# Performance work log

Measured on AMD Instinct MI355X. Metric: run time of the kernel, lower is better.

## Reference

```python
import jax, jax.numpy as jnp
import numpy as np

N = 100000
E = 1600000
B = 64
NUM_CLASSES = 10


def setup_inputs() -> dict:
    key = jax.random.key(0)
    ks = jax.random.split(key, 8)
    x = jax.random.normal(ks[0], (N, 5), dtype=jnp.float32)
    edge_index = jax.random.randint(ks[1], (2, E), 0, N, dtype=jnp.int64)
    batch = jnp.sort(jax.random.randint(ks[2], (N,), 0, B, dtype=jnp.int64))

    def glorot(k, fan_in, fan_out):
        s = jnp.sqrt(6.0 / (fan_in + fan_out)).astype(jnp.float32)
        return jax.random.uniform(k, (fan_in, fan_out), jnp.float32, -s, s)

    dims = [(5, 32), (32, 64), (64, 128), (128, 256)]
    Ws = [glorot(jax.random.fold_in(ks[3], i), a, b) for i, (a, b) in enumerate(dims)]
    bs = [jnp.zeros((b,), jnp.float32) for (_, b) in dims]
    fc1_w = glorot(ks[4], 256, 100)
    fc1_b = jnp.zeros((100,), jnp.float32)
    fc2_w = glorot(ks[5], 100, NUM_CLASSES)
    fc2_b = jnp.zeros((NUM_CLASSES,), jnp.float32)
    return {
        'x': x, 'edge_index': edge_index, 'batch': batch,
        'W1': Ws[0], 'b1': bs[0], 'W2': Ws[1], 'b2': bs[1],
        'W3': Ws[2], 'b3': bs[2], 'W4': Ws[3], 'b4': bs[3],
        'fc1_w': fc1_w, 'fc1_b': fc1_b, 'fc2_w': fc2_w, 'fc2_b': fc2_b,
    }


def _gcn_conv(x, W, b, src, dst, dinv):
    h = x @ W                                   # [N, out]
    norm = (dinv[src] * dinv[dst])[:, None]      # [E, 1]
    msg = h[src] * norm                          # gather + scale
    agg = jax.ops.segment_sum(msg, dst, num_segments=N)
    agg = agg + h * (dinv * dinv)[:, None]       # self-loop contribution
    return agg + b


def reference(x, edge_index, batch, W1, b1, W2, b2, W3, b3, W4, b4,
              fc1_w, fc1_b, fc2_w, fc2_b):
    src, dst = edge_index[0], edge_index[1]
    # degree including self-loop
    deg = jax.ops.segment_sum(jnp.ones((E,), jnp.float32), dst, num_segments=N) + 1.0
    dinv = jax.lax.rsqrt(deg)

    h = jax.nn.relu(_gcn_conv(x, W1, b1, src, dst, dinv))
    # mesh_unpool with pool target 0 -> identity
    h = jax.nn.relu(_gcn_conv(h, W2, b2, src, dst, dinv))
    h = jax.nn.relu(_gcn_conv(h, W3, b3, src, dst, dinv))
    h = jax.nn.relu(_gcn_conv(h, W4, b4, src, dst, dinv))

    # global mean pool over graphs
    sums = jax.ops.segment_sum(h, batch, num_segments=B)
    cnt = jax.ops.segment_sum(jnp.ones((N,), jnp.float32), batch, num_segments=B)
    pooled = sums / jnp.maximum(cnt, 1.0)[:, None]

    h = jax.nn.relu(pooled @ fc1_w + fc1_b)
    return jax.nn.log_softmax(h @ fc2_w + fc2_b, axis=-1)
```

## Files before the change

kernel.cpp:

```cpp
#include <hip/hip_runtime.h>
#include <hip/hip_bf16.h>
#include <cmath>

#define NN 100000
#define NE 1600000
#define NBATCH 64
#define NB 391
#define NBP 512
#define BCAP 5120
#define NPAD (NB * BCAP)

typedef __attribute__((ext_vector_type(8))) _Float16 f16x8;
typedef __attribute__((ext_vector_type(4))) float f32x4;
typedef __attribute__((ext_vector_type(2))) float f32x2;

__device__ __forceinline__ void atomAdd(float* p, float v) {
  unsafeAtomicAdd(p, v);
}

__device__ __forceinline__ unsigned char f2fp8(float f) {
  int pk = __builtin_amdgcn_cvt_pk_fp8_f32(f, f, 0, false);
  return (unsigned char)(pk & 0xff);
}

__global__ __launch_bounds__(256) void k_bin(const int* __restrict__ src,
    const int* __restrict__ dst, int* __restrict__ bucketCnt, unsigned* __restrict__ pairs,
    const float* __restrict__ W2, const float* __restrict__ W3, const float* __restrict__ W4,
    _Float16* __restrict__ Wt2, _Float16* __restrict__ Wt3, _Float16* __restrict__ Wt4) {
  __shared__ int hist[NBP];
  __shared__ int scn[NBP];
  __shared__ int ofs[NBP];
  __shared__ int gbase[NBP];
  __shared__ unsigned buf[4096];
  __shared__ unsigned short bufb[4096];
  const int base = blockIdx.x * 4096;
  const int n = (NE - base < 4096) ? NE - base : 4096;
  for (int i = threadIdx.x; i < NBP; i += 256) hist[i] = 0;
  __syncthreads();

  int myS[16], myD[16];
  int nloc = 0;
  for (int i = threadIdx.x, j = 0; i < n; i += 256, ++j) {
    myS[j] = src[base + i];
    myD[j] = dst[base + i];
    atomicAdd(&hist[myD[j] >> 8], 1);
    nloc = j + 1;
  }
  __syncthreads();

  scn[threadIdx.x] = hist[threadIdx.x];
  scn[threadIdx.x + 256] = hist[threadIdx.x + 256];
  __syncthreads();
  for (int off = 1; off < NBP; off <<= 1) {
    const int i0 = threadIdx.x, i1 = threadIdx.x + 256;
    int t0 = (i0 >= off) ? scn[i0 - off] : 0;
    int t1 = (i1 >= off) ? scn[i1 - off] : 0;
    __syncthreads();
    scn[i0] += t0;
    scn[i1] += t1;
    __syncthreads();
  }
  ofs[threadIdx.x] = scn[threadIdx.x] - hist[threadIdx.x];
  ofs[threadIdx.x + 256] = scn[threadIdx.x + 256] - hist[threadIdx.x + 256];
  for (int b = threadIdx.x; b < NB; b += 256) {
    int c = hist[b];
    if (c) gbase[b] = b * BCAP + atomicAdd(&bucketCnt[b], c);
  }
  __syncthreads();

  for (int j = 0; j < nloc; ++j) {
    int b = myD[j] >> 8;
    int slot = atomicAdd(&ofs[b], 1);
    buf[slot] = ((unsigned)myS[j] << 8) | ((unsigned)myD[j] & 255u);
    bufb[slot] = (unsigned short)b;
  }
  __syncthreads();

  for (int i = threadIdx.x; i < n; i += 256) {
    int b = (int)bufb[i];
    int ex = scn[b] - hist[b];
    pairs[gbase[b] + (i - ex)] = buf[i];
  }

  int idx = blockIdx.x * 256 + threadIdx.x;
  if (idx < 2048) {
    int k = idx / 64, m = idx - k * 64;
    Wt2[m * 32 + k] = (_Float16)W2[idx];
  } else if (idx < 10240) {
    int j = idx - 2048;
    int k = j / 128, m = j - k * 128;
    Wt3[m * 64 + k] = (_Float16)W3[j];
  } else if (idx < 43008) {
    int j = idx - 10240;
    int k = j / 256, m = j - k * 256;
    Wt4[m * 128 + k] = (_Float16)W4[j];
  }
}

__global__ __launch_bounds__(256) void k_cntfill(const unsigned* __restrict__ pairs,
    const int* __restrict__ bucketCnt, const int* __restrict__ batch,
    const float* __restrict__ x, int* __restrict__ rowbeg, int* __restrict__ rowend,
    float* __restrict__ dinv, int* __restrict__ csrc, float* __restrict__ pcnt,
    _Float16* __restrict__ xs8) {
  __shared__ int c[256];
  __shared__ int scn[256];
  __shared__ int rowb[256];
  __shared__ int ofs[256];
  __shared__ int h[64];
  const int tid = threadIdx.x;
  c[tid] = 0; ofs[tid] = 0;
  if (tid < 64) h[tid] = 0;
  __syncthreads();
  const int b = blockIdx.x;
  const int s = b * BCAP;
  const int e = s + bucketCnt[b];
  for (int i = s + tid; i < e; i += 256) atomicAdd(&c[pairs[i] & 255u], 1);
  __syncthreads();
  const int v = c[tid];
  scn[tid] = v;
  __syncthreads();
  for (int off = 1; off < 256; off <<= 1) {
    int t = (tid >= off) ? scn[tid - off] : 0;
    __syncthreads();
    scn[tid] += t;
    __syncthreads();
  }
  rowb[tid] = s + scn[tid] - v;
  const int node = b * 256 + tid;
  rowbeg[node] = rowb[tid];
  rowend[node] = rowb[tid] + v;
  if (node < NN) {
    const float di = rsqrtf((float)v + 1.0f);
    dinv[node] = di;
    f16x8 o = {0, 0, 0, 0, 0, 0, 0, 0};
    o[0] = (_Float16)(x[(size_t)node * 5 + 0] * di);
    o[1] = (_Float16)(x[(size_t)node * 5 + 1] * di);
    o[2] = (_Float16)(x[(size_t)node * 5 + 2] * di);
    o[3] = (_Float16)(x[(size_t)node * 5 + 3] * di);
    o[4] = (_Float16)(x[(size_t)node * 5 + 4] * di);
    *(f16x8*)(xs8 + (size_t)node * 8) = o;
    atomicAdd(&h[batch[node]], 1);
  }
  __syncthreads();
  for (int i = s + tid; i < e; i += 256) {
    unsigned p = pairs[i];
    int t = (int)(p & 255u);
    int pos = rowb[t] + atomicAdd(&ofs[t], 1);
    csrc[pos] = (int)(p >> 8);
  }
  if (tid < 64 && h[tid]) atomAdd(&pcnt[tid], (float)h[tid]);
}

struct MegaArgs {
  const _Float16* xs8;
  const int* rowbeg; const int* rowend; const int* csrc;
  const float* dinv;
  const float* W1; const float* b1;
  unsigned char* F0;
  const _Float16* Wt2; const float* b2;
  unsigned char* F1;
  const _Float16* Wt3; const float* b3;
  unsigned char* F2;
  const _Float16* Wt4; const float* b4;
  _Float16* AG;
  const int* batch; float* pooled; const float* pcnt;
  const float* fc1w; const float* fc1b; const float* fc2w; const float* fc2b;
  float* out;
};

__global__ __launch_bounds__(256) void kw_l1(MegaArgs a) {
  __shared__ float w_s[160];
  __shared__ float b_s[32];
  const int tid = threadIdx.x;
  if (tid < 160) w_s[tid] = a.W1[tid];
  if (tid < 32) b_s[tid] = a.b1[tid];
  __syncthreads();
  const int r = blockIdx.x * 256 + tid;
  if (r >= NN) return;
  const float di = a.dinv[r];
  f16x8 av = *(const f16x8*)(a.xs8 + (size_t)r * 8);
  f16x8 cacc = {0, 0, 0, 0, 0, 0, 0, 0};
  int e = a.rowbeg[r];
  const int e1 = a.rowend[r];
  for (; e + 2 <= e1; e += 2) {
    const int s0 = a.csrc[e], s1 = a.csrc[e + 1];
    av   += *(const f16x8*)(a.xs8 + (size_t)s0 * 8);
    cacc += *(const f16x8*)(a.xs8 + (size_t)s1 * 8);
  }
  if (e < e1) av += *(const f16x8*)(a.xs8 + (size_t)a.csrc[e] * 8);
  av += cacc;
  const float f0 = (float)av[0] * di, f1 = (float)av[1] * di, f2 = (float)av[2] * di,
              f3 = (float)av[3] * di, f4 = (float)av[4] * di;
  float v[32];
#pragma unroll
  for (int j = 0; j < 32; ++j) {
    float s = b_s[j] + f0 * w_s[j] + f1 * w_s[32 + j] + f2 * w_s[64 + j]
                     + f3 * w_s[96 + j] + f4 * w_s[128 + j];
    v[j] = fmaxf(s, 0.f) * di;
  }
  unsigned u[8];
#pragma unroll
  for (int g2 = 0; g2 < 8; ++g2) {
    int uu = 0;
    uu = __builtin_amdgcn_cvt_pk_fp8_f32(v[4 * g2],     v[4 * g2 + 1], uu, false);
    uu = __builtin_amdgcn_cvt_pk_fp8_f32(v[4 * g2 + 2], v[4 * g2 + 3], uu, true);
    u[g2] = (unsigned)uu;
  }
  uint4* op = (uint4*)(a.F0 + (size_t)r * 32);
  op[0] = make_uint4(u[0], u[1], u[2], u[3]);
  op[1] = make_uint4(u[4], u[5], u[6], u[7]);
}

template<int K>
__global__ __launch_bounds__(256) void kw_gather8(const unsigned char* __restrict__ in,
    MegaArgs a) {
  constexpr int TPR = K / 16;
  constexpr int RPB = 256 / TPR;
  const int r = blockIdx.x * RPB + threadIdx.x / TPR;
  if (r >= NN) return;
  const int c = (threadIdx.x % TPR) * 16;
  const float di = a.dinv[r];
  f32x2 acc[8];
  {
    const uint4 v = *(const uint4*)(in + (size_t)r * K + c);
    acc[0] = __builtin_amdgcn_cvt_pk_f32_fp8(v.x, false);
    acc[1] = __builtin_amdgcn_cvt_pk_f32_fp8(v.x, true);
    acc[2] = __builtin_amdgcn_cvt_pk_f32_fp8(v.y, false);
    acc[3] = __builtin_amdgcn_cvt_pk_f32_fp8(v.y, true);
    acc[4] = __builtin_amdgcn_cvt_pk_f32_fp8(v.z, false);
    acc[5] = __builtin_amdgcn_cvt_pk_f32_fp8(v.z, true);
    acc[6] = __builtin_amdgcn_cvt_pk_f32_fp8(v.w, false);
    acc[7] = __builtin_amdgcn_cvt_pk_f32_fp8(v.w, true);
  }
  int e = a.rowbeg[r];
  const int e1 = a.rowend[r];
  for (; e + 2 <= e1; e += 2) {
    const int s0 = a.csrc[e], s1 = a.csrc[e + 1];
    const uint4 v0 = *(const uint4*)(in + (size_t)s0 * K + c);
    const uint4 v1 = *(const uint4*)(in + (size_t)s1 * K + c);
    acc[0] += __builtin_amdgcn_cvt_pk_f32_fp8(v0.x, false);
    acc[1] += __builtin_amdgcn_cvt_pk_f32_fp8(v0.x, true);
    acc[2] += __builtin_amdgcn_cvt_pk_f32_fp8(v0.y, false);
    acc[3] += __builtin_amdgcn_cvt_pk_f32_fp8(v0.y, true);
    acc[4] += __builtin_amdgcn_cvt_pk_f32_fp8(v0.z, false);
    acc[5] += __builtin_amdgcn_cvt_pk_f32_fp8(v0.z, true);
    acc[6] += __builtin_amdgcn_cvt_pk_f32_fp8(v0.w, false);
    acc[7] += __builtin_amdgcn_cvt_pk_f32_fp8(v0.w, true);
    acc[0] += __builtin_amdgcn_cvt_pk_f32_fp8(v1.x, false);
    acc[1] += __builtin_amdgcn_cvt_pk_f32_fp8(v1.x, true);
    acc[2] += __builtin_amdgcn_cvt_pk_f32_fp8(v1.y, false);
    acc[3] += __builtin_amdgcn_cvt_pk_f32_fp8(v1.y, true);
    acc[4] += __builtin_amdgcn_cvt_pk_f32_fp8(v1.z, false);
    acc[5] += __builtin_amdgcn_cvt_pk_f32_fp8(v1.z, true);
    acc[6] += __builtin_amdgcn_cvt_pk_f32_fp8(v1.w, false);
    acc[7] += __builtin_amdgcn_cvt_pk_f32_fp8(v1.w, true);
  }
  if (e < e1) {
    const uint4 v0 = *(const uint4*)(in + (size_t)a.csrc[e] * K + c);
    acc[0] += __builtin_amdgcn_cvt_pk_f32_fp8(v0.x, false);
    acc[1] += __builtin_amdgcn_cvt_pk_f32_fp8(v0.x, true);
    acc[2] += __builtin_amdgcn_cvt_pk_f32_fp8(v0.y, false);
    acc[3] += __builtin_amdgcn_cvt_pk_f32_fp8(v0.y, true);
    acc[4] += __builtin_amdgcn_cvt_pk_f32_fp8(v0.z, false);
    acc[5] += __builtin_amdgcn_cvt_pk_f32_fp8(v0.z, true);
    acc[6] += __builtin_amdgcn_cvt_pk_f32_fp8(v0.w, false);
    acc[7] += __builtin_amdgcn_cvt_pk_f32_fp8(v0.w, true);
  }
  _Float16 o[16];
#pragma unroll
  for (int j = 0; j < 8; ++j) {
    o[2 * j]     = (_Float16)(acc[j].x * di);
    o[2 * j + 1] = (_Float16)(acc[j].y * di);
  }
  uint4* op = (uint4*)(a.AG + (size_t)r * K + c);
  op[0] = *(uint4*)&o[0];
  op[1] = *(uint4*)&o[8];
}

template<int K, int M, int MODE>
__global__ __launch_bounds__(256) void kw_gemm(MegaArgs a,
    const _Float16* __restrict__ Wt, const float* __restrict__ bias,
    unsigned char* __restrict__ outp) {
  constexpr int KC = 32;
  constexpr int KP = K + 8;
  constexpr int WP = KC + 8;
  constexpr int CTW = M / 64;
  constexpr int C8 = K / 8;
  __shared__ _Float16 a_s[64 * KP];
  __shared__ _Float16 w_s[M * WP];
  const int tid = threadIdx.x;
  const int wave = tid >> 6, lane = tid & 63;
  const int m16 = lane & 15, q = lane >> 4;
  const int r0 = blockIdx.x * 64;

  for (int idx = tid; idx < 64 * C8; idx += 256) {
    int row = idx / C8, cc = (idx % C8) * 8;
    uint4 v = {0u, 0u, 0u, 0u};
    if (r0 + row < NN) v = *(const uint4*)(a.AG + (size_t)(r0 + row) * K + cc);
    *(uint4*)&a_s[row * KP + cc] = v;
  }
  f32x4 acc[4][CTW];
#pragma unroll
  for (int rt = 0; rt < 4; ++rt)
#pragma unroll
    for (int ct = 0; ct < CTW; ++ct) acc[rt][ct] = (f32x4){0.f, 0.f, 0.f, 0.f};

  for (int kc = 0; kc < K; kc += KC) {
    __syncthreads();
    for (int idx = tid; idx < M * (KC / 8); idx += 256) {
      int m = idx / (KC / 8), cc = (idx % (KC / 8)) * 8;
      uint4 v = *(const uint4*)(Wt + (size_t)m * K + kc + cc);
      *(uint4*)&w_s[m * WP + cc] = v;
    }
    __syncthreads();
    f16x8 bfr[CTW];
#pragma unroll
    for (int ct = 0; ct < CTW; ++ct)
      bfr[ct] = *(const f16x8*)&w_s[(wave * (M / 4) + ct * 16 + m16) * WP + q * 8];
#pragma unroll
    for (int rt = 0; rt < 4; ++rt) {
      f16x8 afr = *(const f16x8*)&a_s[(rt * 16 + m16) * KP + kc + q * 8];
#pragma unroll
      for (int ct = 0; ct < CTW; ++ct)
        acc[rt][ct] = __builtin_amdgcn_mfma_f32_16x16x32_f16(afr, bfr[ct], acc[rt][ct], 0, 0, 0);
    }
  }

  if constexpr (MODE == 1) {
    const int rlast = (r0 + 63 < NN) ? r0 + 63 : NN - 1;
    const int bmin = a.batch[r0];
    const int bmax = a.batch[rlast];
    int rowb[4][4];
#pragma unroll
    for (int rt = 0; rt < 4; ++rt)
#pragma unroll
      for (int reg = 0; reg < 4; ++reg) {
        const int row = r0 + rt * 16 + q * 4 + reg;
        rowb[rt][reg] = (row < NN) ? a.batch[row] : -1;
      }
#pragma unroll
    for (int ct = 0; ct < CTW; ++ct) {
      const int col = wave * (M / 4) + ct * 16 + m16;
      const float bv = bias[col];
      for (int b = bmin; b <= bmax; ++b) {
        float s = 0.f;
#pragma unroll
        for (int rt = 0; rt < 4; ++rt)
#pragma unroll
          for (int reg = 0; reg < 4; ++reg)
            if (rowb[rt][reg] == b) s += fmaxf(acc[rt][ct][reg] + bv, 0.f);
        s += __shfl_xor(s, 16);
        s += __shfl_xor(s, 32);
        if (q == 0) atomAdd(&a.pooled[b * M + col], s);
      }
    }
  } else {
    float dsc[4][4];
#pragma unroll
    for (int rt = 0; rt < 4; ++rt)
#pragma unroll
      for (int reg = 0; reg < 4; ++reg) {
        const int row = r0 + rt * 16 + q * 4 + reg;
        dsc[rt][reg] = (row < NN) ? a.dinv[row] : 0.f;
      }
#pragma unroll
    for (int rt = 0; rt < 4; ++rt) {
#pragma unroll
      for (int ct = 0; ct < CTW; ++ct) {
        const int col = wave * (M / 4) + ct * 16 + m16;
        const float bv = bias[col];
#pragma unroll
        for (int reg = 0; reg < 4; ++reg) {
          const int row = r0 + rt * 16 + q * 4 + reg;
          if (row < NN) {
            float vv = fmaxf(acc[rt][ct][reg] + bv, 0.f) * dsc[rt][reg];
            outp[(size_t)row * M + col] = f2fp8(vv);
          }
        }
      }
    }
  }
}

__global__ __launch_bounds__(256) void kw_mlp(MegaArgs a) {
  __shared__ float p[256];
  __shared__ float h1[100];
  __shared__ float lo[10];
  const int tid = threadIdx.x;
  const int b = blockIdx.x;
  const float inv = 1.0f / fmaxf(a.pcnt[b], 1.0f);
  p[tid] = a.pooled[b * 256 + tid] * inv;
  __syncthreads();
  for (int j = tid; j < 100; j += 256) {
    float s = a.fc1b[j];
    for (int k = 0; k < 256; ++k) s += p[k] * a.fc1w[k * 100 + j];
    h1[j] = fmaxf(s, 0.f);
  }
  __syncthreads();
  if (tid < 10) {
    float s = a.fc2b[tid];
    for (int k = 0; k < 100; ++k) s += h1[k] * a.fc2w[k * 10 + tid];
    lo[tid] = s;
  }
  __syncthreads();
  if (tid == 0) {
    float m = lo[0];
    for (int j = 1; j < 10; ++j) m = fmaxf(m, lo[j]);
    float ssum = 0.f;
    for (int j = 0; j < 10; ++j) ssum += expf(lo[j] - m);
    float lse = m + logf(ssum);
    for (int j = 0; j < 10; ++j) a.out[b * 10 + j] = lo[j] - lse;
  }
}

extern "C" void kernel_launch(void* const* d_in, const int* in_sizes, int n_in,
                              void* d_out, int out_size, void* d_ws, size_t ws_size,
                              hipStream_t stream) {
  const float* x     = (const float*)d_in[0];
  const int*   ei    = (const int*)d_in[1];
  const int*   batch = (const int*)d_in[2];
  const float* W1 = (const float*)d_in[3];  const float* b1 = (const float*)d_in[4];
  const float* W2 = (const float*)d_in[5];  const float* b2 = (const float*)d_in[6];
  const float* W3 = (const float*)d_in[7];  const float* b3 = (const float*)d_in[8];
  const float* W4 = (const float*)d_in[9];  const float* b4 = (const float*)d_in[10];
  const float* fc1w = (const float*)d_in[11]; const float* fc1b = (const float*)d_in[12];
  const float* fc2w = (const float*)d_in[13]; const float* fc2b = (const float*)d_in[14];
  float* out = (float*)d_out;

  const int* src = ei;
  const int* dst = ei + NE;

  float* ws = (float*)d_ws;
  float* pooled = ws;
  float* pcnt   = pooled + 16384;
  int*   bucketCnt = (int*)(pcnt + 64);
  float* dinv   = (float*)(bucketCnt + 512);
  int*   rowbeg = (int*)(dinv + 100352);
  int*   rowend = rowbeg + 100352;
  int*   csrc   = rowend + 100352;
  unsigned* pairs = (unsigned*)(csrc + NPAD);
  _Float16* xs8 = (_Float16*)(pairs + NPAD);
  unsigned char* F0 = (unsigned char*)(xs8 + 800768);
  unsigned char* F1 = F0 + (size_t)NN * 32;
  unsigned char* F2 = F1 + (size_t)NN * 64;
  _Float16* AG  = (_Float16*)(F2 + (size_t)NN * 128);
  _Float16* Wt2 = AG + (size_t)NN * 128;
  _Float16* Wt3 = Wt2 + 32 * 64;
  _Float16* Wt4 = Wt3 + 64 * 128;

  (void)hipMemsetAsync(pooled, 0, (16384 + 64 + 512) * sizeof(float), stream);
  k_bin<<<(NE + 4095) / 4096, 256, 0, stream>>>(src, dst, bucketCnt, pairs,
                                                W2, W3, W4, Wt2, Wt3, Wt4);
  k_cntfill<<<NB, 256, 0, stream>>>(pairs, bucketCnt, batch, x,
                                    rowbeg, rowend, dinv, csrc, pcnt, xs8);

  MegaArgs m;
  m.xs8 = xs8; m.rowbeg = rowbeg; m.rowend = rowend; m.csrc = csrc;
  m.dinv = dinv;
  m.W1 = W1; m.b1 = b1; m.F0 = F0;
  m.Wt2 = Wt2; m.b2 = b2; m.F1 = F1;
  m.Wt3 = Wt3; m.b3 = b3; m.F2 = F2;
  m.Wt4 = Wt4; m.b4 = b4; m.AG = AG;
  m.batch = batch; m.pooled = pooled; m.pcnt = pcnt;
  m.fc1w = fc1w; m.fc1b = fc1b; m.fc2w = fc2w; m.fc2b = fc2b;
  m.out = out;

  kw_l1<<<(NN + 255) / 256, 256, 0, stream>>>(m);
  kw_gather8<32><<<(NN + 127) / 128, 256, 0, stream>>>(F0, m);
  kw_gemm<32, 64, 0><<<(NN + 63) / 64, 256, 0, stream>>>(m, Wt2, b2, F1);
  kw_gather8<64><<<(NN + 63) / 64, 256, 0, stream>>>(F1, m);
  kw_gemm<64, 128, 0><<<(NN + 63) / 64, 256, 0, stream>>>(m, Wt3, b3, F2);
  kw_gather8<128><<<(NN + 31) / 32, 256, 0, stream>>>(F2, m);
  kw_gemm<128, 256, 1><<<(NN + 63) / 64, 256, 0, stream>>>(m, Wt4, b4, nullptr);
  kw_mlp<<<NBATCH, 256, 0, stream>>>(m);
}
```

Baseline: 285.8 us.

## Store aggregated features in FP8 and fuse MLP head into final GEMM

The gather kernel now writes its aggregated features as packed FP8 instead of FP16, halving the intermediate traffic between gather and GEMM. The GEMM converts FP8 back to FP16 when loading into shared memory. The final GEMM uses a done counter and a release flag so its first 64 blocks spin-wait and then run the MLP and log-softmax, which removes the separate kw_mlp launch. Zeroing of pooled moves into kw_l1, shrinking the memset. Risks are extra FP8 precision loss and possible deadlock if the waiting blocks stay resident while later blocks cannot be scheduled.

```diff
diff --git a/kernel.cpp b/kernel.cpp
--- a/kernel.cpp
+++ b/kernel.cpp
@@ -9,6 +9,7 @@
 #define NBP 512
 #define BCAP 5120
 #define NPAD (NB * BCAP)
+#define FLAG_MAGIC 0x1234567
 
 typedef __attribute__((ext_vector_type(8))) _Float16 f16x8;
 typedef __attribute__((ext_vector_type(4))) float f32x4;
@@ -21,6 +22,18 @@
 __device__ __forceinline__ unsigned char f2fp8(float f) {
   int pk = __builtin_amdgcn_cvt_pk_fp8_f32(f, f, 0, false);
   return (unsigned char)(pk & 0xff);
+}
+
+__device__ __forceinline__ void fp8x16_to_f16(uint4 v, _Float16* h) {
+  f32x2 t;
+  t = __builtin_amdgcn_cvt_pk_f32_fp8(v.x, false); h[0] = (_Float16)t.x;  h[1] = (_Float16)t.y;
+  t = __builtin_amdgcn_cvt_pk_f32_fp8(v.x, true);  h[2] = (_Float16)t.x;  h[3] = (_Float16)t.y;
+  t = __builtin_amdgcn_cvt_pk_f32_fp8(v.y, false); h[4] = (_Float16)t.x;  h[5] = (_Float16)t.y;
+  t = __builtin_amdgcn_cvt_pk_f32_fp8(v.y, true);  h[6] = (_Float16)t.x;  h[7] = (_Float16)t.y;
+  t = __builtin_amdgcn_cvt_pk_f32_fp8(v.z, false); h[8] = (_Float16)t.x;  h[9] = (_Float16)t.y;
+  t = __builtin_amdgcn_cvt_pk_f32_fp8(v.z, true);  h[10] = (_Float16)t.x; h[11] = (_Float16)t.y;
+  t = __builtin_amdgcn_cvt_pk_f32_fp8(v.w, false); h[12] = (_Float16)t.x; h[13] = (_Float16)t.y;
+  t = __builtin_amdgcn_cvt_pk_f32_fp8(v.w, true);  h[14] = (_Float16)t.x; h[15] = (_Float16)t.y;
 }
 
 __global__ __launch_bounds__(256) void k_bin(const int* __restrict__ src,
@@ -162,8 +175,9 @@
   const _Float16* Wt3; const float* b3;
   unsigned char* F2;
   const _Float16* Wt4; const float* b4;
-  _Float16* AG;
+  unsigned char* AG8;
   const int* batch; float* pooled; const float* pcnt;
+  int* done; int* flag;
   const float* fc1w; const float* fc1b; const float* fc2w; const float* fc2b;
   float* out;
 };
@@ -172,6 +186,7 @@
   __shared__ float w_s[160];
   __shared__ float b_s[32];
   const int tid = threadIdx.x;
+  if (blockIdx.x < 64) a.pooled[blockIdx.x * 256 + tid] = 0.f;
   if (tid < 160) w_s[tid] = a.W1[tid];
   if (tid < 32) b_s[tid] = a.b1[tid];
   __syncthreads();
@@ -266,15 +281,17 @@
     acc[6] += __builtin_amdgcn_cvt_pk_f32_fp8(v0.w, false);
     acc[7] += __builtin_amdgcn_cvt_pk_f32_fp8(v0.w, true);
   }
-  _Float16 o[16];
-#pragma unroll
-  for (int j = 0; j < 8; ++j) {
-    o[2 * j]     = (_Float16)(acc[j].x * di);
-    o[2 * j + 1] = (_Float16)(acc[j].y * di);
-  }
-  uint4* op = (uint4*)(a.AG + (size_t)r * K + c);
-  op[0] = *(uint4*)&o[0];
-  op[1] = *(uint4*)&o[8];
+  int w0 = 0, w1 = 0, w2 = 0, w3 = 0;
+  w0 = __builtin_amdgcn_cvt_pk_fp8_f32(acc[0].x * di, acc[0].y * di, 0, false);
+  w0 = __builtin_amdgcn_cvt_pk_fp8_f32(acc[1].x * di, acc[1].y * di, w0, true);
+  w1 = __builtin_amdgcn_cvt_pk_fp8_f32(acc[2].x * di, acc[2].y * di, 0, false);
+  w1 = __builtin_amdgcn_cvt_pk_fp8_f32(acc[3].x * di, acc[3].y * di, w1, true);
+  w2 = __builtin_amdgcn_cvt_pk_fp8_f32(acc[4].x * di, acc[4].y * di, 0, false);
+  w2 = __builtin_amdgcn_cvt_pk_fp8_f32(acc[5].x * di, acc[5].y * di, w2, true);
+  w3 = __builtin_amdgcn_cvt_pk_fp8_f32(acc[6].x * di, acc[6].y * di, 0, false);
+  w3 = __builtin_amdgcn_cvt_pk_fp8_f32(acc[7].x * di, acc[7].y * di, w3, true);
+  *(uint4*)(a.AG8 + (size_t)r * K + c) = make_uint4((unsigned)w0, (unsigned)w1,
+                                                    (unsigned)w2, (unsigned)w3);
 }
 
 template<int K, int M, int MODE>
@@ -285,7 +302,7 @@
   constexpr int KP = K + 8;
   constexpr int WP = KC + 8;
   constexpr int CTW = M / 64;
-  constexpr int C8 = K / 8;
+  constexpr int C16 = K / 16;
   __shared__ _Float16 a_s[64 * KP];
   __shared__ _Float16 w_s[M * WP];
   const int tid = threadIdx.x;
@@ -293,11 +310,14 @@
   const int m16 = lane & 15, q = lane >> 4;
   const int r0 = blockIdx.x * 64;
 
-  for (int idx = tid; idx < 64 * C8; idx += 256) {
-    int row = idx / C8, cc = (idx % C8) * 8;
+  for (int idx = tid; idx < 64 * C16; idx += 256) {
+    int row = idx / C16, cc = (idx % C16) * 16;
     uint4 v = {0u, 0u, 0u, 0u};
-    if (r0 + row < NN) v = *(const uint4*)(a.AG + (size_t)(r0 + row) * K + cc);
-    *(uint4*)&a_s[row * KP + cc] = v;
+    if (r0 + row < NN) v = *(const uint4*)(a.AG8 + (size_t)(r0 + row) * K + cc);
+    _Float16 h[16];
+    fp8x16_to_f16(v, h);
+    *(uint4*)&a_s[row * KP + cc]     = *(uint4*)&h[0];
+    *(uint4*)&a_s[row * KP + cc + 8] = *(uint4*)&h[8];
   }
   f32x4 acc[4][CTW];
 #pragma unroll
@@ -352,6 +372,50 @@
         s += __shfl_xor(s, 16);
         s += __shfl_xor(s, 32);
         if (q == 0) atomAdd(&a.pooled[b * M + col], s);
+      }
+    }
+    __threadfence();
+    __shared__ int ordS;
+    if (tid == 0) ordS = atomicAdd(a.done, 1);
+    __syncthreads();
+    if (ordS == (int)gridDim.x - 1) {
+      __threadfence();
+      if (tid == 0)
+        __hip_atomic_store(a.flag, FLAG_MAGIC, __ATOMIC_RELEASE, __HIP_MEMORY_SCOPE_AGENT);
+    }
+    if (blockIdx.x < NBATCH) {
+      if (tid == 0) {
+        while (__hip_atomic_load(a.flag, __ATOMIC_ACQUIRE, __HIP_MEMORY_SCOPE_AGENT) != FLAG_MAGIC)
+          __builtin_amdgcn_s_sleep(16);
+      }
+      __syncthreads();
+      float* p  = (float*)a_s;
+      float* h1 = p + 256;
+      float* lo = h1 + 104;
+      const int b = blockIdx.x;
+      const float inv = 1.0f / fmaxf(a.pcnt[b], 1.0f);
+      p[tid] = __hip_atomic_load(&a.pooled[b * 256 + tid], __ATOMIC_RELAXED,
+                                 __HIP_MEMORY_SCOPE_AGENT) * inv;
+      __syncthreads();
+      for (int j = tid; j < 100; j += 256) {
+        float s = a.fc1b[j];
+        for (int k = 0; k < 256; ++k) s += p[k] * a.fc1w[k * 100 + j];
+        h1[j] = fmaxf(s, 0.f);
+      }
+      __syncthreads();
+      if (tid < 10) {
+        float s = a.fc2b[tid];
+        for (int k = 0; k < 100; ++k) s += h1[k] * a.fc2w[k * 10 + tid];
+        lo[tid] = s;
+      }
+      __syncthreads();
+      if (tid == 0) {
+        float m = lo[0];
+        for (int j = 1; j < 10; ++j) m = fmaxf(m, lo[j]);
+        float ssum = 0.f;
+        for (int j = 0; j < 10; ++j) ssum += expf(lo[j] - m);
+        float lse = m + logf(ssum);
+        for (int j = 0; j < 10; ++j) a.out[b * 10 + j] = lo[j] - lse;
       }
     }
   } else {
@@ -379,37 +443,6 @@
         }
       }
     }
-  }
-}
-
-__global__ __launch_bounds__(256) void kw_mlp(MegaArgs a) {
-  __shared__ float p[256];
-  __shared__ float h1[100];
-  __shared__ float lo[10];
-  const int tid = threadIdx.x;
-  const int b = blockIdx.x;
-  const float inv = 1.0f / fmaxf(a.pcnt[b], 1.0f);
-  p[tid] = a.pooled[b * 256 + tid] * inv;
-  __syncthreads();
-  for (int j = tid; j < 100; j += 256) {
-    float s = a.fc1b[j];
-    for (int k = 0; k < 256; ++k) s += p[k] * a.fc1w[k * 100 + j];
-    h1[j] = fmaxf(s, 0.f);
-  }
-  __syncthreads();
-  if (tid < 10) {
-    float s = a.fc2b[tid];
-    for (int k = 0; k < 100; ++k) s += h1[k] * a.fc2w[k * 10 + tid];
-    lo[tid] = s;
-  }
-  __syncthreads();
-  if (tid == 0) {
-    float m = lo[0];
-    for (int j = 1; j < 10; ++j) m = fmaxf(m, lo[j]);
-    float ssum = 0.f;
-    for (int j = 0; j < 10; ++j) ssum += expf(lo[j] - m);
-    float lse = m + logf(ssum);
-    for (int j = 0; j < 10; ++j) a.out[b * 10 + j] = lo[j] - lse;
   }
 }
 
@@ -431,24 +464,26 @@
   const int* dst = ei + NE;
 
   float* ws = (float*)d_ws;
-  float* pooled = ws;
-  float* pcnt   = pooled + 16384;
+  float* pcnt      = ws;
   int*   bucketCnt = (int*)(pcnt + 64);
-  float* dinv   = (float*)(bucketCnt + 512);
+  int*   done      = bucketCnt + 512;
+  int*   flag      = done + 1;
+  float* pooled = (float*)(flag + 15);
+  float* dinv   = pooled + 16384;
   int*   rowbeg = (int*)(dinv + 100352);
   int*   rowend = rowbeg + 100352;
   int*   csrc   = rowend + 100352;
   unsigned* pairs = (unsigned*)(csrc + NPAD);
   _Float16* xs8 = (_Float16*)(pairs + NPAD);
   unsigned char* F0 = (unsigned char*)(xs8 + 800768);
-  unsigned char* F1 = F0 + (size_t)NN * 32;
-  unsigned char* F2 = F1 + (size_t)NN * 64;
-  _Float16* AG  = (_Float16*)(F2 + (size_t)NN * 128);
-  _Float16* Wt2 = AG + (size_t)NN * 128;
+  unsigned char* F1 = F0 + 3200000;
+  unsigned char* F2 = F1 + 6400000;
+  unsigned char* AG8 = F2 + 12800000;
+  _Float16* Wt2 = (_Float16*)(AG8 + 12800000);
   _Float16* Wt3 = Wt2 + 32 * 64;
   _Float16* Wt4 = Wt3 + 64 * 128;
 
-  (void)hipMemsetAsync(pooled, 0, (16384 + 64 + 512) * sizeof(float), stream);
+  (void)hipMemsetAsync(ws, 0, 592 * sizeof(float), stream);
   k_bin<<<(NE + 4095) / 4096, 256, 0, stream>>>(src, dst, bucketCnt, pairs,
                                                 W2, W3, W4, Wt2, Wt3, Wt4);
   k_cntfill<<<NB, 256, 0, stream>>>(pairs, bucketCnt, batch, x,
@@ -460,8 +495,9 @@
   m.W1 = W1; m.b1 = b1; m.F0 = F0;
   m.Wt2 = Wt2; m.b2 = b2; m.F1 = F1;
   m.Wt3 = Wt3; m.b3 = b3; m.F2 = F2;
-  m.Wt4 = Wt4; m.b4 = b4; m.AG = AG;
+  m.Wt4 = Wt4; m.b4 = b4; m.AG8 = AG8;
   m.batch = batch; m.pooled = pooled; m.pcnt = pcnt;
+  m.done = done; m.flag = flag;
   m.fc1w = fc1w; m.fc1b = fc1b; m.fc2w = fc2w; m.fc2b = fc2b;
   m.out = out;
 
@@ -472,5 +508,4 @@
   kw_gemm<64, 128, 0><<<(NN + 63) / 64, 256, 0, stream>>>(m, Wt3, b3, F2);
   kw_gather8<128><<<(NN + 31) / 32, 256, 0, stream>>>(F2, m);
   kw_gemm<128, 256, 1><<<(NN + 63) / 64, 256, 0, stream>>>(m, Wt4, b4, nullptr);
-  kw_mlp<<<NBATCH, 256, 0, stream>>>(m);
-}
+}
```

New measurement: 444.0 us. 55.4% more time.
